# Performance work log

Measured on AMD Instinct MI355X. Metric: run time of the kernel, lower is better.

Reference implementation:

```python
import jax, jax.numpy as jnp
import numpy as np

NUM_FRAMES = 6
HEADS = 16
DIM_HEAD = 64


def setup_inputs() -> dict:
    key = jax.random.key(0)
    ks = jax.random.split(key, 7)
    D = 1024
    x = jax.random.normal(ks[0], (12, 1024, D), dtype=jnp.float32)
    context = jax.random.normal(ks[1], (2, 1024, D), dtype=jnp.float32)
    s = 1.0 / np.sqrt(D)
    Wq = jax.random.normal(ks[2], (D, D), dtype=jnp.float32) * s
    Wk = jax.random.normal(ks[3], (D, D), dtype=jnp.float32) * s
    Wv = jax.random.normal(ks[4], (D, D), dtype=jnp.float32) * s
    Wo = jax.random.normal(ks[5], (D, D), dtype=jnp.float32) * s
    bo = jnp.zeros((D,), dtype=jnp.float32)
    return {"x": x, "context": context, "Wq": Wq, "Wk": Wk, "Wv": Wv, "Wo": Wo, "bo": bo}


def reference(x, context, Wq, Wk, Wv, Wo, bo):
    B, S, D = x.shape  # B=12, S=1024, D=1024
    scale = DIM_HEAD ** (-0.5)
    ab = B // NUM_FRAMES  # actual batch after frame inflation
    xr = x.reshape(ab, NUM_FRAMES * S, D)  # [ab, 6144, D]
    # Linear projections (torch Linear: y = x @ W.T)
    q = xr @ Wq.T            # [ab, Sq, inner]
    k = context @ Wk.T       # [ab, Sk, inner]
    v = context @ Wv.T
    Sq = q.shape[1]
    Sk = k.shape[1]
    q = q.reshape(ab, Sq, HEADS, DIM_HEAD).transpose(0, 2, 1, 3)  # [ab,h,Sq,d]
    k = k.reshape(ab, Sk, HEADS, DIM_HEAD).transpose(0, 2, 1, 3)
    v = v.reshape(ab, Sk, HEADS, DIM_HEAD).transpose(0, 2, 1, 3)
    attn = jnp.einsum("bhqd,bhkd->bhqk", q, k) * scale
    attn = jax.nn.softmax(attn, axis=-1)
    out = jnp.einsum("bhqk,bhkd->bhqd", attn, v)
    out = out.transpose(0, 2, 1, 3).reshape(ab, Sq, HEADS * DIM_HEAD)
    out = out @ Wo.T + bo  # dropout is identity at p=0 / eval
    return out.reshape(B, S, D)
```

## Files before the change

### kernel.cpp

```cpp
#include <hip/hip_runtime.h>

typedef short bf16x8 __attribute__((ext_vector_type(8)));
typedef float floatx4 __attribute__((ext_vector_type(4)));
typedef unsigned short u16;
typedef unsigned int u32;

__device__ __forceinline__ u16 f2bf(float f) {
  u32 u = __float_as_uint(f);
  u += 0x7FFF + ((u >> 16) & 1);
  return (u16)(u >> 16);
}
__device__ __forceinline__ u32 packbf(float a, float b) {
  return (u32)f2bf(a) | ((u32)f2bf(b) << 16);
}
__device__ __forceinline__ u32 permpack(u32 a_bits, u32 b_bits) {
  return __builtin_amdgcn_perm(b_bits, a_bits, 0x07060302u);
}

__device__ __forceinline__ float ex2(float x) {
#if __has_builtin(__builtin_amdgcn_exp2f)
  return __builtin_amdgcn_exp2f(x);
#else
  float r;
  asm("v_exp_f32 %0, %1" : "=v"(r) : "v"(x));
  return r;
#endif
}

__device__ __forceinline__ void gload_lds16(const u16* g, u16* l) {
  __builtin_amdgcn_global_load_lds(
      (const __attribute__((address_space(1))) void*)(const void*)g,
      (__attribute__((address_space(3))) void*)(void*)l, 16, 0, 0);
}

__device__ __forceinline__ void bb_stage(const u16* Ag, const u16* Wg,
                                         u16* Asl, u16* Wsl) {
  gload_lds16(Ag, Asl);
  gload_lds16(Ag + 16 * 1024, Asl + 512);
  gload_lds16(Wg, Wsl);
  gload_lds16(Wg + 16 * 1024, Wsl + 512);
}

__device__ __forceinline__ void bb_compute(const u16* As, const u16* Ws,
                                           int wm, int wn, int m16, int quad,
                                           floatx4 acc[4][4]) {
  bf16x8 af[4], bfr[4];
#pragma unroll
  for (int t = 0; t < 4; ++t) {
    af[t]  = *(const bf16x8*)&As[(wm * 64 + t * 16 + m16) * 32 + quad * 8];
    bfr[t] = *(const bf16x8*)&Ws[(wn * 64 + t * 16 + m16) * 32 + quad * 8];
  }
#pragma unroll
  for (int i = 0; i < 4; ++i)
#pragma unroll
    for (int j = 0; j < 4; ++j)
      acc[i][j] = __builtin_amdgcn_mfma_f32_16x16x32_bf16(af[i], bfr[j],
                                                          acc[i][j], 0, 0, 0);
}

__device__ __forceinline__ void bb_mainloop(const u16* __restrict__ A,
                                            const u16* __restrict__ W,
                                            u16* As0, u16* Ws0, u16* As1,
                                            u16* Ws1, int m0, int n0,
                                            floatx4 acc[4][4]) {
  const int tid = threadIdx.x, lane = tid & 63, w = tid >> 6;
  const int wm = w & 1, wn = w >> 1;
  const int m16 = lane & 15, quad = lane >> 4;
  const int lr = lane >> 2;
  const int sc = (lane & 3) * 8;

  const u16* Ag = A + (size_t)(m0 + w * 32 + lr) * 1024 + sc;
  const u16* Wg = W + (size_t)(n0 + w * 32 + lr) * 1024 + sc;
  const int so = (w * 32) * 32;

#pragma unroll
  for (int i = 0; i < 4; ++i)
#pragma unroll
    for (int j = 0; j < 4; ++j) acc[i][j] = (floatx4)0.0f;

  bb_stage(Ag, Wg, As0 + so, Ws0 + so);
  __syncthreads();

  for (int kt = 0; kt < 32; kt += 2) {
    bb_stage(Ag + (kt + 1) * 32, Wg + (kt + 1) * 32, As1 + so, Ws1 + so);
    bb_compute(As0, Ws0, wm, wn, m16, quad, acc);
    __syncthreads();
    if (kt + 2 < 32)
      bb_stage(Ag + (kt + 2) * 32, Wg + (kt + 2) * 32, As0 + so, Ws0 + so);
    bb_compute(As1, Ws1, wm, wn, m16, quad, acc);
    __syncthreads();
  }
}

__global__ __launch_bounds__(256) void gemm_qkv(
    const u16* __restrict__ xb, const u16* __restrict__ ctxb,
    const u16* __restrict__ wqb, const u16* __restrict__ wkb,
    const u16* __restrict__ wvb, u16* __restrict__ Qb, u16* __restrict__ Kbuf,
    u16* __restrict__ Vtb) {
  __shared__ u16 As0[128 * 32];
  __shared__ u16 Ws0[128 * 32];
  __shared__ u16 As1[128 * 32];
  __shared__ u16 Ws1[128 * 32];
  const int lane = threadIdx.x & 63, w = threadIdx.x >> 6;
  const int wm = w & 1, wn = w >> 1;
  const int m16 = lane & 15, quad = lane >> 4;
  const int y = blockIdx.y;
  const u16 *A, *W;
  int m0, mode;
  if (y < 96)       { A = xb;   W = wqb; m0 = y * 128;         mode = 0; }
  else if (y < 112) { A = ctxb; W = wkb; m0 = (y - 96) * 128;  mode = 1; }
  else              { A = ctxb; W = wvb; m0 = (y - 112) * 128; mode = 2; }
  const int n0 = blockIdx.x * 128;
  floatx4 acc[4][4];
  bb_mainloop(A, W, As0, Ws0, As1, Ws1, m0, n0, acc);
  const float cs = (mode == 0) ? 0.18033688011112042f : 1.0f;
#pragma unroll
  for (int j = 0; j < 4; ++j) {
    const int col = n0 + wn * 64 + j * 16 + m16;
#pragma unroll
    for (int i = 0; i < 4; ++i)
#pragma unroll
      for (int r = 0; r < 4; ++r) {
        const int row = m0 + wm * 64 + i * 16 + quad * 4 + r;
        const u16 v = f2bf(acc[i][j][r] * cs);
        if (mode == 0)
          Qb[(size_t)row * 1024 + col] = v;
        else if (mode == 1)
          Kbuf[(size_t)row * 1024 + col] = v;
        else
          Vtb[((size_t)((row >> 10) * 1024 + col)) * 1024 + (row & 1023)] = v;
      }
  }
}

__global__ __launch_bounds__(256) void gemm_out(const u16* __restrict__ A,
                                                const u16* __restrict__ W,
                                                float* __restrict__ C,
                                                const float* __restrict__ bias) {
  __shared__ u16 As0[128 * 32];
  __shared__ u16 Ws0[128 * 32];
  __shared__ u16 As1[128 * 32];
  __shared__ u16 Ws1[128 * 32];
  const int lane = threadIdx.x & 63, w = threadIdx.x >> 6;
  const int wm = w & 1, wn = w >> 1;
  const int m16 = lane & 15, quad = lane >> 4;
  const int n0 = blockIdx.x * 128, m0 = blockIdx.y * 128;
  floatx4 acc[4][4];
  bb_mainloop(A, W, As0, Ws0, As1, Ws1, m0, n0, acc);
#pragma unroll
  for (int j = 0; j < 4; ++j) {
    const int col = n0 + wn * 64 + j * 16 + m16;
    const float bv = bias[col];
#pragma unroll
    for (int i = 0; i < 4; ++i)
#pragma unroll
      for (int r = 0; r < 4; ++r) {
        const int row = m0 + wm * 64 + i * 16 + quad * 4 + r;
        C[(size_t)row * 1024 + col] = acc[i][j][r] + bv;
      }
  }
}

__global__ __launch_bounds__(256) void cvt_all(
    const float* __restrict__ x, const float* __restrict__ ctx,
    const float* __restrict__ wq, const float* __restrict__ wk,
    const float* __restrict__ wv, const float* __restrict__ wo,
    u16* __restrict__ xb, u16* __restrict__ ctxb, u16* __restrict__ wqb,
    u16* __restrict__ wkb, u16* __restrict__ wvb, u16* __restrict__ wob) {
  const u32 i = blockIdx.x * 256 + threadIdx.x;
  const float* s;
  u16* d;
  u32 o;
  if (i < 3145728u)      { s = x;   d = xb;   o = i; }
  else if (i < 3670016u) { s = ctx; d = ctxb; o = i - 3145728u; }
  else if (i < 3932160u) { s = wq;  d = wqb;  o = i - 3670016u; }
  else if (i < 4194304u) { s = wk;  d = wkb;  o = i - 3932160u; }
  else if (i < 4456448u) { s = wv;  d = wvb;  o = i - 4194304u; }
  else                   { s = wo;  d = wob;  o = i - 4456448u; }
  const float4 v = ((const float4*)s)[o];
  uint2 p;
  p.x = packbf(v.x, v.y);
  p.y = packbf(v.z, v.w);
  ((uint2*)d)[o] = p;
}

__global__ __launch_bounds__(256, 4) void attn_flash(
    const u16* __restrict__ Q, const u16* __restrict__ Kb,
    const u16* __restrict__ Vt, u16* __restrict__ O) {
  __shared__ u16 Kl[2 * 64 * 32];
  __shared__ u16 Vl[2 * 64 * 32];
  __shared__ u32 Pl[4 * 32 * 36];
  const int tid = threadIdx.x, lane = tid & 63, w = tid >> 6;
  const int m16 = lane & 15, quad = lane >> 4;
  const int h = blockIdx.y, b = blockIdx.z;
  const int q0 = blockIdx.x * 128 + w * 32;
  u32* const pbase = &Pl[w * 32 * 36];

  bf16x8 aq[2][2];
#pragma unroll
  for (int qt = 0; qt < 2; ++qt)
#pragma unroll
    for (int ks = 0; ks < 2; ++ks)
      aq[qt][ks] =
          *(const bf16x8*)&Q[((size_t)(b * 6144 + q0 + qt * 16 + m16)) * 1024 +
                             h * 64 + ks * 32 + quad * 8];

  const int wk = w & 1, wh = w >> 1;
  const u16* kg = Kb + ((size_t)(b * 1024 + wh * 32 + (lane >> 2))) * 1024 +
                  h * 64 + wk * 32 + (lane & 3) * 8;
  const u16* vg = Vt + ((size_t)(b * 16 + h)) * 65536 +
                  (size_t)(wh * 32 + (lane >> 2)) * 1024 + wk * 32 +
                  (lane & 3) * 8;
  u16* const klb = &Kl[wk * 2048 + wh * 1024];
  u16* const vlb = &Vl[wk * 2048 + wh * 1024];

  bf16x8 vone;
#pragma unroll
  for (int e = 0; e < 8; ++e) vone[e] = (short)0x3F80;

  floatx4 oacc[2][4];
#pragma unroll
  for (int qt = 0; qt < 2; ++qt)
#pragma unroll
    for (int mtd = 0; mtd < 4; ++mtd) oacc[qt][mtd] = (floatx4)0.0f;
  floatx4 lacc[2];
  lacc[0] = (floatx4)0.0f;
  lacc[1] = (floatx4)0.0f;

#pragma unroll 1
  for (int kt = 0; kt < 16; ++kt) {
    gload_lds16(kg, klb);
    gload_lds16(kg + 16 * 1024, klb + 512);
    gload_lds16(vg, vlb);
    gload_lds16(vg + 16 * 1024, vlb + 512);
    kg += 64 * 1024;
    vg += 64;
    __syncthreads();

    floatx4 sst[2][4];
#pragma unroll
    for (int mt = 0; mt < 4; ++mt) {
      const int row = mt * 16 + m16;
      const bf16x8 kf0 = *(const bf16x8*)&Kl[row * 32 + quad * 8];
      const bf16x8 kf1 = *(const bf16x8*)&Kl[2048 + row * 32 + quad * 8];
#pragma unroll
      for (int qt = 0; qt < 2; ++qt) {
        floatx4 t = (floatx4)0.0f;
        t = __builtin_amdgcn_mfma_f32_16x16x32_bf16(kf0, aq[qt][0], t, 0, 0, 0);
        sst[qt][mt] =
            __builtin_amdgcn_mfma_f32_16x16x32_bf16(kf1, aq[qt][1], t, 0, 0, 0);
      }
    }
#pragma unroll
    for (int qt = 0; qt < 2; ++qt) {
      u32* const prow = &pbase[(qt * 16 + m16) * 36 + quad * 2];
#pragma unroll
      for (int mt = 0; mt < 4; ++mt) {
        const u32 b0 = __float_as_uint(ex2(sst[qt][mt][0]));
        const u32 b1 = __float_as_uint(ex2(sst[qt][mt][1]));
        const u32 b2 = __float_as_uint(ex2(sst[qt][mt][2]));
        const u32 b3 = __float_as_uint(ex2(sst[qt][mt][3]));
        uint2 pk;
        pk.x = permpack(b0, b1);
        pk.y = permpack(b2, b3);
        *(uint2*)&prow[mt * 8] = pk;
      }
    }
#pragma unroll
    for (int kk = 0; kk < 2; ++kk) {
      bf16x8 pf[2];
#pragma unroll
      for (int qt = 0; qt < 2; ++qt)
        pf[qt] =
            *(const bf16x8*)&pbase[(qt * 16 + m16) * 36 + kk * 16 + quad * 4];
      lacc[0] = __builtin_amdgcn_mfma_f32_16x16x32_bf16(vone, pf[0], lacc[0],
                                                        0, 0, 0);
      lacc[1] = __builtin_amdgcn_mfma_f32_16x16x32_bf16(vone, pf[1], lacc[1],
                                                        0, 0, 0);
#pragma unroll
      for (int mtd = 0; mtd < 4; ++mtd) {
        const bf16x8 vf =
            *(const bf16x8*)&Vl[kk * 2048 + (mtd * 16 + m16) * 32 + quad * 8];
#pragma unroll
        for (int qt = 0; qt < 2; ++qt)
          oacc[qt][mtd] = __builtin_amdgcn_mfma_f32_16x16x32_bf16(
              vf, pf[qt], oacc[qt][mtd], 0, 0, 0);
      }
    }
    __syncthreads();
  }

#pragma unroll
  for (int qt = 0; qt < 2; ++qt) {
    const float linv = 1.0f / lacc[qt][0];
    const size_t obase =
        ((size_t)(b * 6144 + q0 + qt * 16 + m16)) * 1024 + h * 64;
#pragma unroll
    for (int mtd = 0; mtd < 4; ++mtd) {
      const int d0 = mtd * 16 + quad * 4;
      *(u32*)&O[obase + d0] =
          packbf(oacc[qt][mtd][0] * linv, oacc[qt][mtd][1] * linv);
      *(u32*)&O[obase + d0 + 2] =
          packbf(oacc[qt][mtd][2] * linv, oacc[qt][mtd][3] * linv);
    }
  }
}

template <bool A_BF16, bool OUT_F32, int VT, bool BIAS>
__global__ __launch_bounds__(256) void gemm_nt(
    const void* __restrict__ Ap, const float* __restrict__ W,
    void* __restrict__ Cp, const float* __restrict__ bias, int M, int N,
    int K, float scale) {
  __shared__ u16 As[128 * 40];
  __shared__ u16 Ws[128 * 40];
  const int tid = threadIdx.x;
  const int lane = tid & 63;
  const int wv = tid >> 6;
  const int wm = wv & 1, wn = wv >> 1;
  const int m16 = lane & 15, quad = lane >> 4;
  const int n0 = blockIdx.x * 128;
  const int m0 = blockIdx.y * 128;
  const int lr = tid >> 2;
  const int lc = (tid & 3) * 8;
  floatx4 acc[4][4];
#pragma unroll
  for (int i = 0; i < 4; ++i)
#pragma unroll
    for (int j = 0; j < 4; ++j) acc[i][j] = (floatx4)0.0f;
  const int KT = K >> 5;
  for (int kt = 0; kt < KT; ++kt) {
    const int k0 = kt << 5;
#pragma unroll
    for (int j = 0; j < 2; ++j) {
      const int r = lr + 64 * j;
      if (A_BF16) {
        *(uint4*)&As[r * 40 + lc] =
            *(const uint4*)&((const u16*)Ap)[(size_t)(m0 + r) * K + k0 + lc];
      } else {
        const float* Arow = (const float*)Ap + (size_t)(m0 + r) * K + k0 + lc;
        const float4 a0 = *(const float4*)Arow;
        const float4 a1 = *(const float4*)(Arow + 4);
        uint4 p;
        p.x = packbf(a0.x, a0.y); p.y = packbf(a0.z, a0.w);
        p.z = packbf(a1.x, a1.y); p.w = packbf(a1.z, a1.w);
        *(uint4*)&As[r * 40 + lc] = p;
      }
      const float* Wrow = W + (size_t)(n0 + r) * K + k0 + lc;
      const float4 w0 = *(const float4*)Wrow;
      const float4 w1 = *(const float4*)(Wrow + 4);
      uint4 q;
      q.x = packbf(w0.x, w0.y); q.y = packbf(w0.z, w0.w);
      q.z = packbf(w1.x, w1.y); q.w = packbf(w1.z, w1.w);
      *(uint4*)&Ws[r * 40 + lc] = q;
    }
    __syncthreads();
    bf16x8 af[4], bfr[4];
#pragma unroll
    for (int t = 0; t < 4; ++t) {
      af[t]  = *(const bf16x8*)&As[(wm * 64 + t * 16 + m16) * 40 + quad * 8];
      bfr[t] = *(const bf16x8*)&Ws[(wn * 64 + t * 16 + m16) * 40 + quad * 8];
    }
#pragma unroll
    for (int i = 0; i < 4; ++i)
#pragma unroll
      for (int j = 0; j < 4; ++j)
        acc[i][j] = __builtin_amdgcn_mfma_f32_16x16x32_bf16(af[i], bfr[j],
                                                            acc[i][j], 0, 0, 0);
    __syncthreads();
  }
#pragma unroll
  for (int j = 0; j < 4; ++j) {
    const int col = n0 + wn * 64 + j * 16 + m16;
    const float bv = BIAS ? bias[col] : 0.0f;
#pragma unroll
    for (int i = 0; i < 4; ++i)
#pragma unroll
      for (int r = 0; r < 4; ++r) {
        const int row = m0 + wm * 64 + i * 16 + quad * 4 + r;
        const float v = acc[i][j][r] * scale + bv;
        if (OUT_F32)
          ((float*)Cp)[(size_t)row * N + col] = v;
        else if (VT)
          ((u16*)Cp)[((size_t)((row >> 10) * 1024 + col)) * 1024 +
                     (row & 1023)] = f2bf(v);
        else
          ((u16*)Cp)[(size_t)row * N + col] = f2bf(v);
      }
  }
}

extern "C" void kernel_launch(void* const* d_in, const int* in_sizes, int n_in,
                              void* d_out, int out_size, void* d_ws,
                              size_t ws_size, hipStream_t stream) {
  const float* x   = (const float*)d_in[0];
  const float* ctx = (const float*)d_in[1];
  const float* Wq  = (const float*)d_in[2];
  const float* Wk  = (const float*)d_in[3];
  const float* Wv  = (const float*)d_in[4];
  const float* Wo  = (const float*)d_in[5];
  const float* bo  = (const float*)d_in[6];
  float* out = (float*)d_out;
  const dim3 blk(256);
  const float CS = 0.18033688011112042f;

  u16* Qb   = (u16*)d_ws;
  u16* Kbuf = Qb + 12582912;
  u16* Vtb  = Kbuf + 2097152;
  u16* Obx  = Vtb + 2097152;
  u16* ctxb = Obx + 12582912;
  u16* wqb  = ctxb + 2097152;
  u16* wkb  = wqb + 1048576;
  u16* wvb  = wkb + 1048576;
  u16* wob  = wvb + 1048576;
  const size_t need = (size_t)(wob + 1048576 - Qb) * sizeof(u16);

  if (ws_size >= need) {
    cvt_all<<<18432, blk, 0, stream>>>(x, ctx, Wq, Wk, Wv, Wo, Obx, ctxb, wqb,
                                       wkb, wvb, wob);
    gemm_qkv<<<dim3(8, 128), blk, 0, stream>>>(Obx, ctxb, wqb, wkb, wvb, Qb,
                                               Kbuf, Vtb);
    attn_flash<<<dim3(48, 16, 2), blk, 0, stream>>>(Qb, Kbuf, Vtb, Obx);
    gemm_out<<<dim3(8, 96), blk, 0, stream>>>(Obx, wob, out, bo);
  } else {
    gemm_nt<false, false, 0, false><<<dim3(8, 96), blk, 0, stream>>>(
        x, Wq, Qb, nullptr, 12288, 1024, 1024, CS);
    gemm_nt<false, false, 0, false><<<dim3(8, 16), blk, 0, stream>>>(
        ctx, Wk, Kbuf, nullptr, 2048, 1024, 1024, 1.0f);
    gemm_nt<false, false, 1, false><<<dim3(8, 16), blk, 0, stream>>>(
        ctx, Wv, Vtb, nullptr, 2048, 1024, 1024, 1.0f);
    attn_flash<<<dim3(48, 16, 2), blk, 0, stream>>>(Qb, Kbuf, Vtb, Obx);
    gemm_nt<true, true, 0, true><<<dim3(8, 96), blk, 0, stream>>>(
        Obx, Wo, out, bo, 12288, 1024, 1024, 1.0f);
  }
}
```

Before: 297.6 us.

## Swizzle workgroup ids across XCDs and hoist LDS fragment loads before staging

Remaps block indices in the QKV GEMM, output GEMM and flash attention kernels so that consecutive work tiles land on the same XCD. This is meant to improve L2 reuse of the shared weight and K/V tiles. The GEMM main loop is also split so LDS fragment reads are issued before the next global-to-LDS stage, with sched_barriers pinning the order of reads, prefetch and MFMA. The remap assumes the grid sizes (1024, 768, 1536 blocks) divide by 8, and the barriers reduce the compiler's freedom to interleave instructions.

Result: no change. 299.2 us (+0.5%).

```diff
diff --git a/kernel.cpp b/kernel.cpp
--- a/kernel.cpp
+++ b/kernel.cpp
@@ -33,6 +33,11 @@
       (__attribute__((address_space(3))) void*)(void*)l, 16, 0, 0);
 }
 
+__device__ __forceinline__ int xcd_swz(int disp, int nwg) {
+  const int q = nwg >> 3;
+  return (disp & 7) * q + (disp >> 3);
+}
+
 __device__ __forceinline__ void bb_stage(const u16* Ag, const u16* Wg,
                                          u16* Asl, u16* Wsl) {
   gload_lds16(Ag, Asl);
@@ -41,15 +46,18 @@
   gload_lds16(Wg + 16 * 1024, Wsl + 512);
 }
 
-__device__ __forceinline__ void bb_compute(const u16* As, const u16* Ws,
-                                           int wm, int wn, int m16, int quad,
-                                           floatx4 acc[4][4]) {
-  bf16x8 af[4], bfr[4];
+__device__ __forceinline__ void bb_frags(const u16* As, const u16* Ws, int wm,
+                                         int wn, int m16, int quad,
+                                         bf16x8 af[4], bf16x8 bfr[4]) {
 #pragma unroll
   for (int t = 0; t < 4; ++t) {
     af[t]  = *(const bf16x8*)&As[(wm * 64 + t * 16 + m16) * 32 + quad * 8];
     bfr[t] = *(const bf16x8*)&Ws[(wn * 64 + t * 16 + m16) * 32 + quad * 8];
   }
+}
+
+__device__ __forceinline__ void bb_mfma(const bf16x8 af[4], const bf16x8 bfr[4],
+                                        floatx4 acc[4][4]) {
 #pragma unroll
   for (int i = 0; i < 4; ++i)
 #pragma unroll
@@ -81,13 +89,20 @@
   bb_stage(Ag, Wg, As0 + so, Ws0 + so);
   __syncthreads();
 
+  bf16x8 af[4], bfr[4];
   for (int kt = 0; kt < 32; kt += 2) {
+    bb_frags(As0, Ws0, wm, wn, m16, quad, af, bfr);
+    __builtin_amdgcn_sched_barrier(0);
     bb_stage(Ag + (kt + 1) * 32, Wg + (kt + 1) * 32, As1 + so, Ws1 + so);
-    bb_compute(As0, Ws0, wm, wn, m16, quad, acc);
-    __syncthreads();
+    __builtin_amdgcn_sched_barrier(0);
+    bb_mfma(af, bfr, acc);
+    __syncthreads();
+    bb_frags(As1, Ws1, wm, wn, m16, quad, af, bfr);
+    __builtin_amdgcn_sched_barrier(0);
     if (kt + 2 < 32)
       bb_stage(Ag + (kt + 2) * 32, Wg + (kt + 2) * 32, As0 + so, Ws0 + so);
-    bb_compute(As1, Ws1, wm, wn, m16, quad, acc);
+    __builtin_amdgcn_sched_barrier(0);
+    bb_mfma(af, bfr, acc);
     __syncthreads();
   }
 }
@@ -104,13 +119,15 @@
   const int lane = threadIdx.x & 63, w = threadIdx.x >> 6;
   const int wm = w & 1, wn = w >> 1;
   const int m16 = lane & 15, quad = lane >> 4;
-  const int y = blockIdx.y;
+  const int disp = blockIdx.y * 8 + blockIdx.x;
+  const int work = xcd_swz(disp, 1024);
+  const int y = work >> 3;
+  const int n0 = (work & 7) * 128;
   const u16 *A, *W;
   int m0, mode;
   if (y < 96)       { A = xb;   W = wqb; m0 = y * 128;         mode = 0; }
   else if (y < 112) { A = ctxb; W = wkb; m0 = (y - 96) * 128;  mode = 1; }
   else              { A = ctxb; W = wvb; m0 = (y - 112) * 128; mode = 2; }
-  const int n0 = blockIdx.x * 128;
   floatx4 acc[4][4];
   bb_mainloop(A, W, As0, Ws0, As1, Ws1, m0, n0, acc);
   const float cs = (mode == 0) ? 0.18033688011112042f : 1.0f;
@@ -144,7 +161,9 @@
   const int lane = threadIdx.x & 63, w = threadIdx.x >> 6;
   const int wm = w & 1, wn = w >> 1;
   const int m16 = lane & 15, quad = lane >> 4;
-  const int n0 = blockIdx.x * 128, m0 = blockIdx.y * 128;
+  const int disp = blockIdx.y * 8 + blockIdx.x;
+  const int work = xcd_swz(disp, 768);
+  const int n0 = (work & 7) * 128, m0 = (work >> 3) * 128;
   floatx4 acc[4][4];
   bb_mainloop(A, W, As0, Ws0, As1, Ws1, m0, n0, acc);
 #pragma unroll
@@ -192,8 +211,13 @@
   __shared__ u32 Pl[4 * 32 * 36];
   const int tid = threadIdx.x, lane = tid & 63, w = tid >> 6;
   const int m16 = lane & 15, quad = lane >> 4;
-  const int h = blockIdx.y, b = blockIdx.z;
-  const int q0 = blockIdx.x * 128 + w * 32;
+  const int disp =
+      blockIdx.x + 48 * (blockIdx.y + 16 * blockIdx.z);
+  const int work = xcd_swz(disp, 1536);
+  const int qx = work % 48;
+  const int bh = work / 48;
+  const int h = bh & 15, b = bh >> 4;
+  const int q0 = qx * 128 + w * 32;
   u32* const pbase = &Pl[w * 32 * 36];
 
   bf16x8 aq[2][2];
```
